# Kernel optimization log

Measured on AMD Instinct MI355X. Metric: run time of the kernel, lower is better.

Reference implementation:

```python
import jax, jax.numpy as jnp
import numpy as np

B, T, H, N = 2, 1024, 32, 64
HN = H * N              # 2048 hidden size
KVH, KVD = 8, 512       # GQA kv heads / kv width; repeat = HN // KVD = 4
LW, LA, LV, LG, LK = 64, 64, 32, 128, 32   # wavgk_split_list
EPS = 1e-6

def _rms(x, w):
    xf = x.astype(jnp.float32)
    var = jnp.mean(xf * xf, axis=-1, keepdims=True)
    return (w * (xf * jax.lax.rsqrt(var + EPS))).astype(x.dtype)

def _rot_half(x):
    x1, x2 = jnp.split(x, 2, axis=-1)
    return jnp.concatenate([-x2, x1], axis=-1)

def setup_inputs():
    key = jax.random.key(0)
    ks = iter(jax.random.split(key, 32))
    nrm = lambda s, sc=1.0: jax.random.normal(next(ks), s, jnp.float32) * sc
    d = {
        'x_in': nrm((B, T, HN)),
        'v_first': nrm((B, T, KVH, N)),
        'k_first': nrm((B, T, KVH, N)),
        'state': jnp.zeros((B, H, N, N), jnp.float32),
    }
    pos = jnp.arange(T, dtype=jnp.float32)
    inv = 1.0 / (10000.0 ** (jnp.arange(0, N, 2, dtype=jnp.float32) / N))
    ang = pos[:, None] * inv[None, :]
    ang = jnp.concatenate([ang, ang], axis=-1)   # [T, N]
    d['calc_cos'] = jnp.broadcast_to(jnp.cos(ang), (B, T, N))
    d['calc_sin'] = jnp.broadcast_to(jnp.sin(ang), (B, T, N))
    d.update(
        wavgk1=nrm((HN, LW + LA + LV + LG + LK), 0.02),
        w0=jnp.zeros((HN,), jnp.float32), w2=nrm((LW, HN), 0.02),
        a0=jnp.zeros((HN,), jnp.float32), a2=nrm((LA, HN), 0.02),
        v0=jnp.zeros((KVD,), jnp.float32), v2=nrm((LV, KVD), 0.02),
        g2=nrm((LG, HN), 0.02),
        k0=jnp.zeros((KVD,), jnp.float32), k2=nrm((LK, KVD), 0.02),
        r_k=nrm((H, N), 0.1),
        RKV_w=nrm((HN + 2 * KVD, HN), 0.02),
        O_w=nrm((HN, HN), 0.02),
        R_bias=jnp.zeros((HN,), jnp.float32),
        K_bias=jnp.zeros((KVD,), jnp.float32),
        V_bias=jnp.zeros((KVD,), jnp.float32),
        O_bias=jnp.zeros((HN,), jnp.float32),
        ln_r=jnp.ones((N,), jnp.float32),
        ln_k=jnp.ones((N,), jnp.float32),
        ln1=jnp.ones((HN,), jnp.float32),
    )
    return d

def reference(x_in, v_first, k_first, state, calc_cos, calc_sin, wavgk1, w0, w2,
              a0, a2, v0, v2, g2, k0, k2, r_k, RKV_w, O_w, R_bias, K_bias,
              V_bias, O_bias, ln_r, ln_k, ln1):
    rep = HN // KVD
    x = _rms(x_in, ln1)
    rkv = x @ RKV_w.T                                   # dense form of fpx_matmul
    r, k, v = jnp.split(rkv, [HN, HN + KVD], axis=-1)
    xw, xa, xv, xg, xk = jnp.split(x @ wavgk1, [LW, LW + LA, LW + LA + LV, LW + LA + LV + LG], axis=-1)
    r = r + R_bias; k = k + K_bias; v = v + V_bias
    r = _rms(r.reshape(B, T, H, N), ln_r)
    k = _rms(k.reshape(B, T, KVH, N), ln_k)
    cos, sin = calc_cos[:, :, None, :], calc_sin[:, :, None, :]   # unsqueeze_dim=2
    r = r * cos + _rot_half(r) * sin
    k = k * cos + _rot_half(k) * sin
    v = v.reshape(B, T, KVH, N)
    # layer_id > 0 path: gated residual toward layer-0 v/k
    gate_v = jax.nn.sigmoid(xv @ v2 + v0).reshape(B, T, KVH, N)
    v = v + (v_first - v) * gate_v
    gate_k = jax.nn.sigmoid(xk @ k2 + k0).reshape(B, T, KVH, N)
    k = k + (k_first - k) * gate_k
    w = jnp.tanh(xw) @ w2 + w0
    w = -jax.nn.softplus(-w) - 0.5
    # GQA repeat kv heads to H
    k = jnp.broadcast_to(k[:, :, :, None, :], (B, T, KVH, rep, N)).reshape(B, T, HN)
    v = jnp.broadcast_to(v[:, :, :, None, :], (B, T, KVH, rep, N)).reshape(B, T, HN)
    r = r.reshape(B, T, HN)
    a = jax.nn.sigmoid(xa @ a2 + a0)
    g = jax.nn.sigmoid(xg) @ g2
    kh = k.reshape(B, T, H, N)
    kk = (kh / jnp.maximum(jnp.linalg.norm(kh, axis=-1, keepdims=True), 1e-12)).reshape(B, T, HN)
    k = k * (1.0 - w + a)
    aa, bb = -kk, kk * a
    w = -jnp.exp(w.astype(jnp.float32))                 # log-decay (negative)
    # RWKV-7 recurrence: S <- S*diag(exp(w)) + (S a) b^T + v k^T ; o = S r
    hv = lambda t: jnp.moveaxis(t.reshape(B, T, H, N).astype(jnp.float32), 1, 0)
    def step(S, ts):
        r_t, w_t, k_t, v_t, a_t, b_t = ts               # each [B,H,N]
        sa = jnp.einsum('bhvk,bhk->bhv', S, a_t)
        S = S * jnp.exp(w_t)[:, :, None, :] + sa[..., None] * b_t[:, :, None, :] + v_t[..., None] * k_t[:, :, None, :]
        return S, jnp.einsum('bhvk,bhk->bhv', S, r_t)
    _, o = jax.lax.scan(step, state.astype(jnp.float32), (hv(r), hv(w), hv(k), hv(v), hv(aa), hv(bb)))
    xx = jnp.moveaxis(o, 0, 1).reshape(B, T, HN) * float(N) ** -0.5
    r_, k_, v_ = (t.reshape(B, T, H, N) for t in (r, k, v))
    bonus = (jnp.sum(r_ * k_ * r_k, axis=-1, keepdims=True) * v_).reshape(B, T, HN)
    xx = xx.astype(x_in.dtype) + bonus
    return x_in + (xx * g) @ O_w.T + O_bias
```

## Files before the change

### kernel.cpp

```cpp
#include <hip/hip_runtime.h>
#include <hip/hip_bf16.h>

#define B_ 2
#define T_ 1024
#define H_ 32
#define N_ 64
#define HN_ 2048
#define KVH_ 8
#define KVD_ 512
#define MTOK 2048
#define SMN 7168
#define KCAT 320
#define CH 64
#define NCH 16
#define NCHUNK 1024

typedef __bf16 bf16x8 __attribute__((ext_vector_type(8)));
typedef float f32x4 __attribute__((ext_vector_type(4)));
typedef float f32x2 __attribute__((ext_vector_type(2)));

__device__ __forceinline__ float sigmf(float x) { return 1.f / (1.f + expf(-x)); }

__global__ void f2b_kernel(const float* __restrict__ in, __hip_bfloat16* __restrict__ out, int n) {
    int i = blockIdx.x * 256 + threadIdx.x;
    if (i < n) out[i] = __float2bfloat16(in[i]);
}

__global__ void transpose_f2b_kernel(const float* __restrict__ in, __hip_bfloat16* __restrict__ out,
                                     int rows, int cols) {
    long i = (long)blockIdx.x * 256 + threadIdx.x;
    if (i >= (long)rows * cols) return;
    int c = (int)(i / rows), r = (int)(i % rows);
    out[i] = __float2bfloat16(in[(size_t)r * cols + c]);
}

__global__ void build_wcat_kernel(const float* __restrict__ w2, const float* __restrict__ a2,
                                  const float* __restrict__ v2, const float* __restrict__ g2,
                                  const float* __restrict__ k2, __hip_bfloat16* __restrict__ out) {
    long i = (long)blockIdx.x * 256 + threadIdx.x;
    if (i >= (long)SMN * KCAT) return;
    int j = (int)(i / KCAT), k = (int)(i % KCAT);
    float v = 0.f;
    if (j < 2048)      { if (k < 64)             v = w2[(size_t)k * 2048 + j]; }
    else if (j < 4096) { if (k >= 64 && k < 128)  v = a2[(size_t)(k - 64) * 2048 + (j - 2048)]; }
    else if (j < 4608) { if (k >= 128 && k < 160) v = v2[(size_t)(k - 128) * 512 + (j - 4096)]; }
    else if (j < 6656) { if (k >= 160 && k < 288) v = g2[(size_t)(k - 160) * 2048 + (j - 4608)]; }
    else               { if (k >= 288)            v = k2[(size_t)(k - 288) * 512 + (j - 6656)]; }
    out[i] = __float2bfloat16(v);
}

__global__ __launch_bounds__(256) void rmsnorm_kernel(const float* __restrict__ x,
                                                      const float* __restrict__ ln1,
                                                      __hip_bfloat16* __restrict__ out) {
    const int bt = blockIdx.x, tid = threadIdx.x;
    const float* row = x + (size_t)bt * HN_;
    float4 v0 = *(const float4*)(row + tid * 8);
    float4 v1 = *(const float4*)(row + tid * 8 + 4);
    float s = v0.x*v0.x + v0.y*v0.y + v0.z*v0.z + v0.w*v0.w
            + v1.x*v1.x + v1.y*v1.y + v1.z*v1.z + v1.w*v1.w;
    for (int m = 1; m < 64; m <<= 1) s += __shfl_xor(s, m);
    __shared__ float red[4];
    if ((tid & 63) == 0) red[tid >> 6] = s;
    __syncthreads();
    s = red[0] + red[1] + red[2] + red[3];
    float scale = rsqrtf(s * (1.f / HN_) + 1e-6f);
    float vals[8] = {v0.x, v0.y, v0.z, v0.w, v1.x, v1.y, v1.z, v1.w};
    #pragma unroll
    for (int j = 0; j < 8; ++j)
        out[(size_t)bt * HN_ + tid * 8 + j] = __float2bfloat16(vals[j] * scale * ln1[tid * 8 + j]);
}

__global__ void xwmod_kernel(const float* __restrict__ in, __hip_bfloat16* __restrict__ out) {
    long i = (long)blockIdx.x * 256 + threadIdx.x;
    if (i >= (long)MTOK * KCAT) return;
    int c = (int)(i % KCAT);
    float x = in[i];
    if (c < 64) x = tanhf(x);
    else if (c >= 160 && c < 288) x = sigmf(x);
    out[i] = __float2bfloat16(x);
}

__global__ __launch_bounds__(256) void gemm_bt(const __hip_bfloat16* __restrict__ A,
                                               const __hip_bfloat16* __restrict__ B,
                                               float* __restrict__ C, int M, int N, int K,
                                               const float* __restrict__ bias,
                                               const float* __restrict__ addend) {
    __shared__ __align__(16) __hip_bfloat16 As[64][40];
    __shared__ __align__(16) __hip_bfloat16 Bs[64][40];
    const int tid = threadIdx.x;
    const int wave = tid >> 6, lane = tid & 63;
    const int wr = (wave >> 1) * 32, wc = (wave & 1) * 32;
    const int brow = blockIdx.y << 6, bcol = blockIdx.x << 6;
    const int lrow = tid >> 2, lcol = (tid & 3) << 3;
    const int fr = lane & 15, ko = (lane >> 4) << 3;
    f32x4 acc[2][2] = {};
    for (int k0 = 0; k0 < K; k0 += 32) {
        uint4 av = *(const uint4*)(A + (size_t)(brow + lrow) * K + k0 + lcol);
        uint4 bv = *(const uint4*)(B + (size_t)(bcol + lrow) * K + k0 + lcol);
        *(uint4*)(&As[lrow][lcol]) = av;
        *(uint4*)(&Bs[lrow][lcol]) = bv;
        __syncthreads();
        bf16x8 af0 = *(const bf16x8*)(&As[wr + fr][ko]);
        bf16x8 af1 = *(const bf16x8*)(&As[wr + 16 + fr][ko]);
        bf16x8 bf0 = *(const bf16x8*)(&Bs[wc + fr][ko]);
        bf16x8 bf1 = *(const bf16x8*)(&Bs[wc + 16 + fr][ko]);
        acc[0][0] = __builtin_amdgcn_mfma_f32_16x16x32_bf16(af0, bf0, acc[0][0], 0, 0, 0);
        acc[0][1] = __builtin_amdgcn_mfma_f32_16x16x32_bf16(af0, bf1, acc[0][1], 0, 0, 0);
        acc[1][0] = __builtin_amdgcn_mfma_f32_16x16x32_bf16(af1, bf0, acc[1][0], 0, 0, 0);
        acc[1][1] = __builtin_amdgcn_mfma_f32_16x16x32_bf16(af1, bf1, acc[1][1], 0, 0, 0);
        __syncthreads();
    }
    const int cr = (lane >> 4) << 2, cc = lane & 15;
    #pragma unroll
    for (int i = 0; i < 2; ++i)
        #pragma unroll
        for (int j = 0; j < 2; ++j)
            #pragma unroll
            for (int r = 0; r < 4; ++r) {
                int row = brow + wr + i * 16 + cr + r;
                int col = bcol + wc + j * 16 + cc;
                float v = acc[i][j][r];
                if (bias) v += bias[col];
                if (addend) v += addend[(size_t)row * N + col];
                C[(size_t)row * N + col] = v;
            }
}

__global__ __launch_bounds__(256) void gemm_bt128(const __hip_bfloat16* __restrict__ A,
                                                  const __hip_bfloat16* __restrict__ B,
                                                  float* __restrict__ C, int M, int N, int K,
                                                  const float* __restrict__ bias,
                                                  const float* __restrict__ addend) {
    __shared__ __align__(16) __hip_bfloat16 As[128][40];
    __shared__ __align__(16) __hip_bfloat16 Bs[128][40];
    const int tid = threadIdx.x;
    const int wave = tid >> 6, lane = tid & 63;
    const int wr = (wave >> 1) * 64, wc = (wave & 1) * 64;
    const int brow = blockIdx.y << 7, bcol = blockIdx.x << 7;
    const int lrow = tid >> 2, lcol = (tid & 3) << 3;
    const int fr = lane & 15, ko = (lane >> 4) << 3;
    f32x4 acc[4][4] = {};
    const __hip_bfloat16* Ap = A + (size_t)(brow + lrow) * K + lcol;
    const __hip_bfloat16* Bp = B + (size_t)(bcol + lrow) * K + lcol;
    const size_t half = (size_t)64 * K;
    for (int k0 = 0; k0 < K; k0 += 32) {
        uint4 a0 = *(const uint4*)(Ap + k0);
        uint4 a1 = *(const uint4*)(Ap + half + k0);
        uint4 b0 = *(const uint4*)(Bp + k0);
        uint4 b1 = *(const uint4*)(Bp + half + k0);
        *(uint4*)(&As[lrow][lcol]) = a0;
        *(uint4*)(&As[lrow + 64][lcol]) = a1;
        *(uint4*)(&Bs[lrow][lcol]) = b0;
        *(uint4*)(&Bs[lrow + 64][lcol]) = b1;
        __syncthreads();
        bf16x8 af[4], bfr[4];
        #pragma unroll
        for (int i = 0; i < 4; ++i) {
            af[i]  = *(const bf16x8*)(&As[wr + i * 16 + fr][ko]);
            bfr[i] = *(const bf16x8*)(&Bs[wc + i * 16 + fr][ko]);
        }
        #pragma unroll
        for (int i = 0; i < 4; ++i)
            #pragma unroll
            for (int j = 0; j < 4; ++j)
                acc[i][j] = __builtin_amdgcn_mfma_f32_16x16x32_bf16(af[i], bfr[j], acc[i][j], 0, 0, 0);
        __syncthreads();
    }
    const int cr = (lane >> 4) << 2, cc = lane & 15;
    #pragma unroll
    for (int i = 0; i < 4; ++i)
        #pragma unroll
        for (int j = 0; j < 4; ++j) {
            const int row0 = brow + wr + i * 16 + cr;
            const int col = bcol + wc + j * 16 + cc;
            #pragma unroll
            for (int r = 0; r < 4; ++r) {
                float v = acc[i][j][r];
                if (bias) v += bias[col];
                if (addend) v += addend[(size_t)(row0 + r) * N + col];
                C[(size_t)(row0 + r) * N + col] = v;
            }
        }
}

__global__ __launch_bounds__(256) void compose_kernel(
    const float* __restrict__ RKV, const float* __restrict__ SM,
    const float* __restrict__ v_first, const float* __restrict__ k_first,
    const float* __restrict__ cosd, const float* __restrict__ sind,
    const float* __restrict__ R_bias, const float* __restrict__ K_bias,
    const float* __restrict__ V_bias, const float* __restrict__ w0,
    const float* __restrict__ a0, const float* __restrict__ v0b,
    const float* __restrict__ k0b, const float* __restrict__ ln_r,
    const float* __restrict__ ln_k, const float* __restrict__ r_k,
    char* __restrict__ SC, __hip_bfloat16* __restrict__ VB, float* __restrict__ SB) {
    __shared__ __align__(16) float rbuf[HN_];
    __shared__ __align__(16) float kbuf[KVD_];
    __shared__ __align__(16) float vbuf[KVD_];
    __shared__ float knorms[KVH_];
    __shared__ float cosb[64], sinb[64];
    const int bt = blockIdx.x;
    const int b = bt >> 10, t = bt & 1023;
    const int tid = threadIdx.x;
    const float* rkvrow = RKV + (size_t)bt * 3072;
    const float* smrow = SM + (size_t)bt * SMN;

    if (tid < 64) {
        cosb[tid] = cosd[(size_t)bt * 64 + tid];
        sinb[tid] = sind[(size_t)bt * 64 + tid];
    }

    const int h = tid >> 3;
    const int off = (tid & 7) << 3;
    const int n0 = tid << 3;
    float rraw[8];
    {
        float4 x0 = *(const float4*)(rkvrow + n0);
        float4 x1 = *(const float4*)(rkvrow + n0 + 4);
        float4 b0 = *(const float4*)(R_bias + n0);
        float4 b1 = *(const float4*)(R_bias + n0 + 4);
        rraw[0] = x0.x + b0.x; rraw[1] = x0.y + b0.y; rraw[2] = x0.z + b0.z; rraw[3] = x0.w + b0.w;
        rraw[4] = x1.x + b1.x; rraw[5] = x1.y + b1.y; rraw[6] = x1.z + b1.z; rraw[7] = x1.w + b1.w;
    }
    float rss = 0.f;
    #pragma unroll
    for (int j = 0; j < 8; ++j) { rss += rraw[j] * rraw[j]; rbuf[n0 + j] = rraw[j]; }
    rss += __shfl_xor(rss, 1); rss += __shfl_xor(rss, 2); rss += __shfl_xor(rss, 4);
    float rscale = rsqrtf(rss * (1.f / 64.f) + 1e-6f);

    const int kvh = tid >> 5;
    const int ko2 = (tid & 31) << 1;
    const int kidx = kvh * 64 + ko2;
    float kraw0 = rkvrow[2048 + kidx] + K_bias[kidx];
    float kraw1 = rkvrow[2048 + kidx + 1] + K_bias[kidx + 1];
    float kss = kraw0 * kraw0 + kraw1 * kraw1;
    kss += __shfl_xor(kss, 1); kss += __shfl_xor(kss, 2); kss += __shfl_xor(kss, 4);
    kss += __shfl_xor(kss, 8); kss += __shfl_xor(kss, 16);
    float kscale = rsqrtf(kss * (1.f / 64.f) + 1e-6f);
    kbuf[kidx] = kraw0; kbuf[kidx + 1] = kraw1;

    {
        float va = rkvrow[2560 + kidx] + V_bias[kidx];
        float vb2 = rkvrow[2560 + kidx + 1] + V_bias[kidx + 1];
        float gv0 = sigmf(smrow[4096 + kidx] + v0b[kidx]);
        float gv1 = sigmf(smrow[4096 + kidx + 1] + v0b[kidx + 1]);
        vbuf[kidx] = va + (v_first[(size_t)bt * 512 + kidx] - va) * gv0;
        vbuf[kidx + 1] = vb2 + (v_first[(size_t)bt * 512 + kidx + 1] - vb2) * gv1;
    }
    __syncthreads();

    float rf[8];
    #pragma unroll
    for (int j = 0; j < 8; ++j) {
        int nn = off + j;
        int nn2 = (nn + 32) & 63;
        float val = rbuf[h * 64 + nn] * rscale * ln_r[nn];
        float oth = rbuf[h * 64 + nn2] * rscale * ln_r[nn2];
        float rot = (nn < 32) ? -oth : oth;
        rf[j] = val * cosb[nn] + rot * sinb[nn];
    }
    float kfv[2];
    #pragma unroll
    for (int j = 0; j < 2; ++j) {
        int nn = ko2 + j;
        int nn2 = (nn + 32) & 63;
        float val = kbuf[kvh * 64 + nn] * kscale * ln_k[nn];
        float oth = kbuf[kvh * 64 + nn2] * kscale * ln_k[nn2];
        float rot = (nn < 32) ? -oth : oth;
        float kr = val * cosb[nn] + rot * sinb[nn];
        float gk = sigmf(smrow[6656 + kvh * 64 + nn] + k0b[kvh * 64 + nn]);
        kfv[j] = kr + (k_first[(size_t)bt * 512 + kvh * 64 + nn] - kr) * gk;
    }
    __syncthreads();
    kbuf[kidx] = kfv[0]; kbuf[kidx + 1] = kfv[1];
    float kn = kfv[0] * kfv[0] + kfv[1] * kfv[1];
    kn += __shfl_xor(kn, 1); kn += __shfl_xor(kn, 2); kn += __shfl_xor(kn, 4);
    kn += __shfl_xor(kn, 8); kn += __shfl_xor(kn, 16);
    if ((tid & 31) == 0) knorms[kvh] = fmaxf(sqrtf(kn), 1e-12f);
    __syncthreads();

    const float knv = knorms[h >> 2];
    char* scb = SC + ((size_t)(b * H_ + h) * T_ + t) * 896;
    __hip_bfloat16* us = (__hip_bfloat16*)scb;
    float* df = (float*)(scb + 640);
    float4 w1a = *(const float4*)(smrow + n0);
    float4 w1b = *(const float4*)(smrow + n0 + 4);
    float4 ara = *(const float4*)(smrow + 2048 + n0);
    float4 arb = *(const float4*)(smrow + 2048 + n0 + 4);
    float w1arr[8] = {w1a.x, w1a.y, w1a.z, w1a.w, w1b.x, w1b.y, w1b.z, w1b.w};
    float aarr[8] = {ara.x, ara.y, ara.z, ara.w, arb.x, arb.y, arb.z, arb.w};
    float bsum = 0.f;
    #pragma unroll
    for (int j = 0; j < 8; ++j) {
        int nn = off + j, n = n0 + j;
        float w1 = w1arr[j] + w0[n];
        float w2v = -log1pf(expf(-w1)) - 0.5f;
        float av = sigmf(aarr[j] + a0[n]);
        float dec = expf(-expf(w2v));
        float kb = kbuf[(h >> 2) * 64 + nn];
        float vbv = vbuf[(h >> 2) * 64 + nn];
        float kkv = kb / knv;
        float ksc = kb * (1.f - w2v + av);
        us[nn]       = __float2bfloat16(rf[j]);
        us[64 + nn]  = __float2bfloat16(ksc);
        us[128 + nn] = __float2bfloat16(-kkv);
        us[192 + nn] = __float2bfloat16(kkv * av);
        us[256 + nn] = __float2bfloat16(vbv);
        df[nn] = dec;
        VB[(size_t)bt * HN_ + n] = __float2bfloat16(vbv);
        bsum += rf[j] * ksc * r_k[h * 64 + nn];
    }
    bsum += __shfl_xor(bsum, 1); bsum += __shfl_xor(bsum, 2); bsum += __shfl_xor(bsum, 4);
    if ((tid & 7) == 0) SB[bt * H_ + h] = bsum;
}

__global__ __launch_bounds__(256) void scan_pass1(
    const char* __restrict__ SC, float* __restrict__ Q, float* __restrict__ O,
    float* __restrict__ Pf, float* __restrict__ Sf) {
    const int chunk = blockIdx.x;
    const int bh = chunk >> 4, c = chunk & 15;
    const int b = bh >> 5, h = bh & 31;
    const int tid = threadIdx.x;
    const int wid = tid >> 6, lane = tid & 63;
    const int mat = wid >> 1;
    const int rhalf = wid & 1;
    const int row = rhalf * 32 + (lane & 31);
    const int chalf = lane >> 5;
    const int cb = chalf * 32;
    const char* base = SC + ((size_t)bh * T_ + (size_t)c * CH) * 896;
    __shared__ __align__(16) float ld[2][5][64];

    f32x4 R4[8];
    #pragma unroll
    for (int j = 0; j < 8; ++j)
        #pragma unroll
        for (int e = 0; e < 4; ++e)
            R4[j][e] = (mat == 0 && cb + 4 * j + e == row) ? 1.f : 0.f;

    float p0, p1;
    auto LOADT = [&](int t) {
        const __hip_bfloat16* us = (const __hip_bfloat16*)(base + (size_t)t * 896);
        if (wid == 0)      { p0 = __bfloat162float(us[128 + lane]); p1 = __bfloat162float(us[lane]); }
        else if (wid == 1) { p0 = __bfloat162float(us[192 + lane]); p1 = 0.f; }
        else if (wid == 2) { p0 = *(const float*)(base + (size_t)t * 896 + 640 + 4 * lane);
                             p1 = __bfloat162float(us[256 + (lane & 31)]); }
        else               { p0 = __bfloat162float(us[64 + lane]);
                             p1 = __bfloat162float(us[256 + 32 + (lane & 31)]); }
    };
    LOADT(0);
    float* qrow = Q + (size_t)chunk * CH * 64 + row;
    float* orow = O + ((size_t)b * T_ + (size_t)c * CH) * HN_ + h * 64 + row;
    for (int t = 0; t < CH; ++t) {
        const int buf = t & 1;
        float vt = p1;
        if (wid == 0)      { ld[buf][0][lane] = p0; ld[buf][4][lane] = p1; }
        else if (wid == 1) { ld[buf][1][lane] = p0; }
        else if (wid == 2) { ld[buf][2][lane] = p0; }
        else               { ld[buf][3][lane] = p0; }
        __syncthreads();
        if (t + 1 < CH) LOADT(t + 1);
        f32x4 da = {0,0,0,0}, db = {0,0,0,0};
        #pragma unroll
        for (int j = 0; j < 8; j += 2) {
            da += R4[j]     * *(const f32x4*)&ld[buf][0][cb + 4 * j];
            db += R4[j + 1] * *(const f32x4*)&ld[buf][0][cb + 4 * j + 4];
        }
        float dot = da[0] + da[1] + da[2] + da[3] + db[0] + db[1] + db[2] + db[3];
        dot += __shfl_xor(dot, 32);
        const f32x4 dotv = {dot, dot, dot, dot};
        f32x4 qa = {0,0,0,0}, qb = {0,0,0,0};
        if (mat == 0) {
            #pragma unroll
            for (int j = 0; j < 8; j += 2) {
                f32x4 d0 = *(const f32x4*)&ld[buf][2][cb + 4 * j];
                f32x4 b0 = *(const f32x4*)&ld[buf][1][cb + 4 * j];
                f32x4 r0 = *(const f32x4*)&ld[buf][4][cb + 4 * j];
                f32x4 Pn = R4[j] * d0 + dotv * b0;
                R4[j] = Pn; qa += Pn * r0;
                f32x4 d1 = *(const f32x4*)&ld[buf][2][cb + 4 * j + 4];
                f32x4 b1 = *(const f32x4*)&ld[buf][1][cb + 4 * j + 4];
                f32x4 r1 = *(const f32x4*)&ld[buf][4][cb + 4 * j + 4];
                f32x4 Pm = R4[j + 1] * d1 + dotv * b1;
                R4[j + 1] = Pm; qb += Pm * r1;
            }
            float qs = qa[0]+qa[1]+qa[2]+qa[3]+qb[0]+qb[1]+qb[2]+qb[3];
            qs += __shfl_xor(qs, 32);
            if (chalf == 0) qrow[(size_t)t * 64] = qs;
        } else {
            const f32x4 vtv = {vt, vt, vt, vt};
            #pragma unroll
            for (int j = 0; j < 8; j += 2) {
                f32x4 d0 = *(const f32x4*)&ld[buf][2][cb + 4 * j];
                f32x4 b0 = *(const f32x4*)&ld[buf][1][cb + 4 * j];
                f32x4 k0 = *(const f32x4*)&ld[buf][3][cb + 4 * j];
                f32x4 r0 = *(const f32x4*)&ld[buf][4][cb + 4 * j];
                f32x4 Sn = R4[j] * d0 + dotv * b0 + vtv * k0;
                R4[j] = Sn; qa += Sn * r0;
                f32x4 d1 = *(const f32x4*)&ld[buf][2][cb + 4 * j + 4];
                f32x4 b1 = *(const f32x4*)&ld[buf][1][cb + 4 * j + 4];
                f32x4 k1 = *(const f32x4*)&ld[buf][3][cb + 4 * j + 4];
                f32x4 r1 = *(const f32x4*)&ld[buf][4][cb + 4 * j + 4];
                f32x4 Sm = R4[j + 1] * d1 + dotv * b1 + vtv * k1;
                R4[j + 1] = Sm; qb += Sm * r1;
            }
            float os = qa[0]+qa[1]+qa[2]+qa[3]+qb[0]+qb[1]+qb[2]+qb[3];
            os += __shfl_xor(os, 32);
            if (chalf == 0) orow[(size_t)t * HN_] = os;
        }
    }
    float* fp = (mat == 0 ? Pf : Sf) + (size_t)chunk * 4096 + (size_t)row * 64 + cb;
    #pragma unroll
    for (int j = 0; j < 8; ++j)
        *(f32x4*)(fp + 4 * j) = R4[j];
}

__global__ __launch_bounds__(256) void scan_pass2(
    const float* __restrict__ Pf, float* __restrict__ Sf, const float* __restrict__ state) {
    const int blk = blockIdx.x;
    const int bh = blk >> 2, rb = blk & 3;
    const int tid = threadIdx.x;
    const int lv = tid >> 4, c0 = (tid & 15) << 2;
    __shared__ __align__(16) float S[16][68];
    __shared__ __align__(16) float P[64][64];

    *(f32x4*)&S[lv][c0] = *(const f32x4*)&state[(size_t)bh * 4096 + 1024 * rb + tid * 4];
    const size_t pbase = (size_t)(bh * NCH) * 4096;
    {
        f32x4 p0[4];
        #pragma unroll
        for (int j = 0; j < 4; ++j) p0[j] = *(const f32x4*)&Pf[pbase + tid * 16 + 4 * j];
        #pragma unroll
        for (int j = 0; j < 4; ++j) *(f32x4*)(&P[0][0] + tid * 16 + 4 * j) = p0[j];
    }
    __syncthreads();

    for (int c = 0; c < NCH; ++c) {
        const size_t ck = (size_t)(bh * NCH + c) * 4096;
        f32x4 pp[4];
        if (c + 1 < NCH) {
            #pragma unroll
            for (int j = 0; j < 4; ++j) pp[j] = *(const f32x4*)&Pf[ck + 4096 + tid * 16 + 4 * j];
        }
        f32x4 acc = *(const f32x4*)&Sf[ck + 1024 * rb + tid * 4];
        f32x4 cur = *(const f32x4*)&S[lv][c0];
        #pragma unroll 4
        for (int k4 = 0; k4 < 64; k4 += 4) {
            f32x4 sk4 = *(const f32x4*)&S[lv][k4];
            #pragma unroll
            for (int kk = 0; kk < 4; ++kk) {
                f32x4 pr = *(const f32x4*)&P[k4 + kk][c0];
                f32x4 sv = {sk4[kk], sk4[kk], sk4[kk], sk4[kk]};
                acc += sv * pr;
            }
        }
        __syncthreads();
        *(f32x4*)&S[lv][c0] = acc;
        if (c + 1 < NCH) {
            #pragma unroll
            for (int j = 0; j < 4; ++j) *(f32x4*)(&P[0][0] + tid * 16 + 4 * j) = pp[j];
        }
        *(f32x4*)&Sf[ck + 1024 * rb + tid * 4] = cur;
        __syncthreads();
    }
}

__global__ __launch_bounds__(64) void scan_pass3(
    const float* __restrict__ Q, const float* __restrict__ Sinit, float* __restrict__ O) {
    const int chunk = blockIdx.x;
    const int bh = chunk >> 4, c = chunk & 15;
    const int b = bh >> 5, h = bh & 31;
    const int t = threadIdx.x;
    __shared__ __align__(16) float S[64][64];
    #pragma unroll
    for (int j = 0; j < 16; ++j)
        *(f32x4*)&S[t][4 * j] = *(const f32x4*)&Sinit[(size_t)chunk * 4096 + (size_t)t * 64 + 4 * j];
    __syncthreads();
    float q[64];
    #pragma unroll
    for (int j = 0; j < 16; ++j)
        *(f32x4*)&q[4 * j] = *(const f32x4*)&Q[((size_t)chunk * CH + t) * 64 + 4 * j];
    float* orow = O + ((size_t)b * T_ + (size_t)c * CH + t) * HN_ + h * 64;
    #pragma unroll 4
    for (int v = 0; v < 64; ++v) {
        f32x4 a = {0, 0, 0, 0};
        #pragma unroll
        for (int j = 0; j < 16; ++j)
            a += *(const f32x4*)&S[v][4 * j] * *(const f32x4*)&q[4 * j];
        orow[v] = (a[0] + a[1] + a[2] + a[3] + orow[v]) * 0.125f;
    }
}

__global__ void post_kernel(const float* __restrict__ O, const float* __restrict__ SB,
                            const __hip_bfloat16* __restrict__ VB, const float* __restrict__ SM,
                            __hip_bfloat16* __restrict__ Ub) {
    long i = (long)blockIdx.x * 256 + threadIdx.x;
    if (i >= (long)MTOK * HN_) return;
    int bt = (int)(i >> 11), n = (int)(i & 2047), h = n >> 6;
    float u = (O[i] + SB[bt * H_ + h] * __bfloat162float(VB[i])) * SM[(size_t)bt * SMN + 4608 + n];
    Ub[i] = __float2bfloat16(u);
}

extern "C" void kernel_launch(void* const* d_in, const int* in_sizes, int n_in,
                              void* d_out, int out_size, void* d_ws, size_t ws_size,
                              hipStream_t stream) {
    (void)in_sizes; (void)n_in; (void)out_size; (void)ws_size;
    const float* x_in    = (const float*)d_in[0];
    const float* v_first = (const float*)d_in[1];
    const float* k_first = (const float*)d_in[2];
    const float* state   = (const float*)d_in[3];
    const float* calc_cos= (const float*)d_in[4];
    const float* calc_sin= (const float*)d_in[5];
    const float* wavgk1  = (const float*)d_in[6];
    const float* w0      = (const float*)d_in[7];
    const float* w2      = (const float*)d_in[8];
    const float* a0      = (const float*)d_in[9];
    const float* a2      = (const float*)d_in[10];
    const float* v0      = (const float*)d_in[11];
    const float* v2      = (const float*)d_in[12];
    const float* g2      = (const float*)d_in[13];
    const float* k0      = (const float*)d_in[14];
    const float* k2      = (const float*)d_in[15];
    const float* r_k     = (const float*)d_in[16];
    const float* RKV_w   = (const float*)d_in[17];
    const float* O_w     = (const float*)d_in[18];
    const float* R_bias  = (const float*)d_in[19];
    const float* K_bias  = (const float*)d_in[20];
    const float* V_bias  = (const float*)d_in[21];
    const float* O_bias  = (const float*)d_in[22];
    const float* ln_r    = (const float*)d_in[23];
    const float* ln_k    = (const float*)d_in[24];
    const float* ln1     = (const float*)d_in[25];
    float* out = (float*)d_out;

    char* ws = (char*)d_ws;
    size_t off = 0;
    auto alloc = [&](size_t bytes) -> char* {
        char* p = ws + off;
        off = (off + bytes + 255) & ~(size_t)255;
        return p;
    };
    float* SMf = (float*)alloc((size_t)MTOK * SMN * 4);
    char*  SCb = alloc((size_t)64 * T_ * 896);
    __hip_bfloat16* Ub = (__hip_bfloat16*)SCb;
    __hip_bfloat16* VBb = (__hip_bfloat16*)alloc((size_t)MTOK * HN_ * 2);
    float* SBf = (float*)alloc((size_t)MTOK * H_ * 4);
    float* Of  = (float*)alloc((size_t)MTOK * HN_ * 4);
    __hip_bfloat16* OWb = (__hip_bfloat16*)alloc((size_t)2048 * 2048 * 2);

    size_t ovl = off;
    __hip_bfloat16* Xb     = (__hip_bfloat16*)alloc((size_t)MTOK * HN_ * 2);
    __hip_bfloat16* RKVb   = (__hip_bfloat16*)alloc((size_t)3072 * 2048 * 2);
    __hip_bfloat16* WT1b   = (__hip_bfloat16*)alloc((size_t)320 * 2048 * 2);
    __hip_bfloat16* Wcatb  = (__hip_bfloat16*)alloc((size_t)SMN * KCAT * 2);
    __hip_bfloat16* XWmodb = (__hip_bfloat16*)alloc((size_t)MTOK * KCAT * 2);
    float* RKVf  = (float*)alloc((size_t)MTOK * 3072 * 4);
    float* XWraw = (float*)alloc((size_t)MTOK * KCAT * 4);
    off = ovl;
    float* Qf  = (float*)alloc((size_t)NCHUNK * CH * 64 * 4);
    float* Pff = (float*)alloc((size_t)NCHUNK * 4096 * 4);
    float* Sff = (float*)alloc((size_t)NCHUNK * 4096 * 4);

    f2b_kernel<<<(3072 * 2048 + 255) / 256, 256, 0, stream>>>(RKV_w, RKVb, 3072 * 2048);
    f2b_kernel<<<(2048 * 2048 + 255) / 256, 256, 0, stream>>>(O_w, OWb, 2048 * 2048);
    transpose_f2b_kernel<<<(320 * 2048 + 255) / 256, 256, 0, stream>>>(wavgk1, WT1b, 2048, 320);
    build_wcat_kernel<<<(SMN * KCAT + 255) / 256, 256, 0, stream>>>(w2, a2, v2, g2, k2, Wcatb);

    rmsnorm_kernel<<<MTOK, 256, 0, stream>>>(x_in, ln1, Xb);

    gemm_bt128<<<dim3(3072 / 128, MTOK / 128), 256, 0, stream>>>(Xb, RKVb, RKVf, MTOK, 3072, 2048, nullptr, nullptr);
    gemm_bt<<<dim3(320 / 64, MTOK / 64), 256, 0, stream>>>(Xb, WT1b, XWraw, MTOK, 320, 2048, nullptr, nullptr);
    xwmod_kernel<<<(MTOK * KCAT + 255) / 256, 256, 0, stream>>>(XWraw, XWmodb);
    gemm_bt128<<<dim3(SMN / 128, MTOK / 128), 256, 0, stream>>>(XWmodb, Wcatb, SMf, MTOK, SMN, KCAT, nullptr, nullptr);

    compose_kernel<<<MTOK, 256, 0, stream>>>(RKVf, SMf, v_first, k_first, calc_cos, calc_sin,
                                             R_bias, K_bias, V_bias, w0, a0, v0, k0,
                                             ln_r, ln_k, r_k, SCb, VBb, SBf);

    scan_pass1<<<NCHUNK, 256, 0, stream>>>(SCb, Qf, Of, Pff, Sff);
    scan_pass2<<<B_ * H_ * 4, 256, 0, stream>>>(Pff, Sff, state);
    scan_pass3<<<NCHUNK, 64, 0, stream>>>(Qf, Sff, Of);

    post_kernel<<<(MTOK * HN_ + 255) / 256, 256, 0, stream>>>(Of, SBf, VBb, SMf, Ub);
    gemm_bt128<<<dim3(HN_ / 128, MTOK / 128), 256, 0, stream>>>(Ub, OWb, out, MTOK, HN_, 2048, O_bias, x_in);
}
```

Before: 459.0 us.

## Halve scan chunk size, merge prep kernels, fuse pass3 with post gating

Scan chunk length drops from 64 to 32, doubling the number of chunks so more blocks run in the parallel scan passes. The four weight-conversion kernels are merged into one prep launch. The gate values are written as bf16 by the compose kernel, so the SM buffer can move into the overlapped workspace region. The separate post kernel is folded into scan pass3, which now produces the gated bf16 output directly, removing one full pass over the fp32 output. The trade-off is more per-chunk state traffic in pass1, pass2 and pass3, and an extra bf16 gate buffer.

```diff
diff --git a/kernel.cpp b/kernel.cpp
--- a/kernel.cpp
+++ b/kernel.cpp
@@ -11,9 +11,9 @@
 #define MTOK 2048
 #define SMN 7168
 #define KCAT 320
-#define CH 64
-#define NCH 16
-#define NCHUNK 1024
+#define CH 32
+#define NCH 32
+#define NCHUNK 2048
 
 typedef __bf16 bf16x8 __attribute__((ext_vector_type(8)));
 typedef float f32x4 __attribute__((ext_vector_type(4)));
@@ -21,24 +21,29 @@
 
 __device__ __forceinline__ float sigmf(float x) { return 1.f / (1.f + expf(-x)); }
 
-__global__ void f2b_kernel(const float* __restrict__ in, __hip_bfloat16* __restrict__ out, int n) {
-    int i = blockIdx.x * 256 + threadIdx.x;
-    if (i < n) out[i] = __float2bfloat16(in[i]);
-}
-
-__global__ void transpose_f2b_kernel(const float* __restrict__ in, __hip_bfloat16* __restrict__ out,
-                                     int rows, int cols) {
+#define PREP_N1 (3072 * 2048)
+#define PREP_N2 (2048 * 2048)
+#define PREP_N3 (320 * 2048)
+#define PREP_N4 (SMN * KCAT)
+__global__ void prep_kernel(const float* __restrict__ RKV_w, const float* __restrict__ O_w,
+                            const float* __restrict__ wavgk1,
+                            const float* __restrict__ w2, const float* __restrict__ a2,
+                            const float* __restrict__ v2, const float* __restrict__ g2,
+                            const float* __restrict__ k2,
+                            __hip_bfloat16* __restrict__ RKVb, __hip_bfloat16* __restrict__ OWb,
+                            __hip_bfloat16* __restrict__ WT1b, __hip_bfloat16* __restrict__ Wcatb) {
     long i = (long)blockIdx.x * 256 + threadIdx.x;
-    if (i >= (long)rows * cols) return;
-    int c = (int)(i / rows), r = (int)(i % rows);
-    out[i] = __float2bfloat16(in[(size_t)r * cols + c]);
-}
-
-__global__ void build_wcat_kernel(const float* __restrict__ w2, const float* __restrict__ a2,
-                                  const float* __restrict__ v2, const float* __restrict__ g2,
-                                  const float* __restrict__ k2, __hip_bfloat16* __restrict__ out) {
-    long i = (long)blockIdx.x * 256 + threadIdx.x;
-    if (i >= (long)SMN * KCAT) return;
+    if (i < PREP_N1) { RKVb[i] = __float2bfloat16(RKV_w[i]); return; }
+    i -= PREP_N1;
+    if (i < PREP_N2) { OWb[i] = __float2bfloat16(O_w[i]); return; }
+    i -= PREP_N2;
+    if (i < PREP_N3) {
+        int c = (int)(i / 2048), r = (int)(i % 2048);
+        WT1b[i] = __float2bfloat16(wavgk1[(size_t)r * 320 + c]);
+        return;
+    }
+    i -= PREP_N3;
+    if (i >= PREP_N4) return;
     int j = (int)(i / KCAT), k = (int)(i % KCAT);
     float v = 0.f;
     if (j < 2048)      { if (k < 64)             v = w2[(size_t)k * 2048 + j]; }
@@ -46,7 +51,7 @@
     else if (j < 4608) { if (k >= 128 && k < 160) v = v2[(size_t)(k - 128) * 512 + (j - 4096)]; }
     else if (j < 6656) { if (k >= 160 && k < 288) v = g2[(size_t)(k - 160) * 2048 + (j - 4608)]; }
     else               { if (k >= 288)            v = k2[(size_t)(k - 288) * 512 + (j - 6656)]; }
-    out[i] = __float2bfloat16(v);
+    Wcatb[i] = __float2bfloat16(v);
 }
 
 __global__ __launch_bounds__(256) void rmsnorm_kernel(const float* __restrict__ x,
@@ -192,7 +197,8 @@
     const float* __restrict__ a0, const float* __restrict__ v0b,
     const float* __restrict__ k0b, const float* __restrict__ ln_r,
     const float* __restrict__ ln_k, const float* __restrict__ r_k,
-    char* __restrict__ SC, __hip_bfloat16* __restrict__ VB, float* __restrict__ SB) {
+    char* __restrict__ SC, __hip_bfloat16* __restrict__ VB, float* __restrict__ SB,
+    __hip_bfloat16* __restrict__ G) {
     __shared__ __align__(16) float rbuf[HN_];
     __shared__ __align__(16) float kbuf[KVD_];
     __shared__ __align__(16) float vbuf[KVD_];
@@ -286,8 +292,11 @@
     float4 w1b = *(const float4*)(smrow + n0 + 4);
     float4 ara = *(const float4*)(smrow + 2048 + n0);
     float4 arb = *(const float4*)(smrow + 2048 + n0 + 4);
+    float4 ga  = *(const float4*)(smrow + 4608 + n0);
+    float4 gb  = *(const float4*)(smrow + 4608 + n0 + 4);
     float w1arr[8] = {w1a.x, w1a.y, w1a.z, w1a.w, w1b.x, w1b.y, w1b.z, w1b.w};
     float aarr[8] = {ara.x, ara.y, ara.z, ara.w, arb.x, arb.y, arb.z, arb.w};
+    float garr[8] = {ga.x, ga.y, ga.z, ga.w, gb.x, gb.y, gb.z, gb.w};
     float bsum = 0.f;
     #pragma unroll
     for (int j = 0; j < 8; ++j) {
@@ -307,6 +316,7 @@
         us[256 + nn] = __float2bfloat16(vbv);
         df[nn] = dec;
         VB[(size_t)bt * HN_ + n] = __float2bfloat16(vbv);
+        G[(size_t)bt * HN_ + n] = __float2bfloat16(garr[j]);
         bsum += rf[j] * ksc * r_k[h * 64 + nn];
     }
     bsum += __shfl_xor(bsum, 1); bsum += __shfl_xor(bsum, 2); bsum += __shfl_xor(bsum, 4);
@@ -317,7 +327,7 @@
     const char* __restrict__ SC, float* __restrict__ Q, float* __restrict__ O,
     float* __restrict__ Pf, float* __restrict__ Sf) {
     const int chunk = blockIdx.x;
-    const int bh = chunk >> 4, c = chunk & 15;
+    const int bh = chunk >> 5, c = chunk & 31;
     const int b = bh >> 5, h = bh & 31;
     const int tid = threadIdx.x;
     const int wid = tid >> 6, lane = tid & 63;
@@ -463,40 +473,41 @@
     }
 }
 
-__global__ __launch_bounds__(64) void scan_pass3(
-    const float* __restrict__ Q, const float* __restrict__ Sinit, float* __restrict__ O) {
+__global__ __launch_bounds__(64) void pass3_post(
+    const float* __restrict__ Q, const float* __restrict__ Sinit, const float* __restrict__ OL,
+    const float* __restrict__ SB, const __hip_bfloat16* __restrict__ VB,
+    const __hip_bfloat16* __restrict__ G, __hip_bfloat16* __restrict__ Ub) {
     const int chunk = blockIdx.x;
-    const int bh = chunk >> 4, c = chunk & 15;
+    const int bh = chunk >> 5, c = chunk & 31;
     const int b = bh >> 5, h = bh & 31;
-    const int t = threadIdx.x;
+    const int tid = threadIdx.x;
     __shared__ __align__(16) float S[64][64];
     #pragma unroll
     for (int j = 0; j < 16; ++j)
-        *(f32x4*)&S[t][4 * j] = *(const f32x4*)&Sinit[(size_t)chunk * 4096 + (size_t)t * 64 + 4 * j];
+        *(f32x4*)&S[tid][4 * j] = *(const f32x4*)&Sinit[(size_t)chunk * 4096 + (size_t)tid * 64 + 4 * j];
     __syncthreads();
+    const int t = tid >> 1, vh = (tid & 1) << 5;
+    const size_t bt = (size_t)b * T_ + (size_t)c * CH + t;
     float q[64];
     #pragma unroll
     for (int j = 0; j < 16; ++j)
         *(f32x4*)&q[4 * j] = *(const f32x4*)&Q[((size_t)chunk * CH + t) * 64 + 4 * j];
-    float* orow = O + ((size_t)b * T_ + (size_t)c * CH + t) * HN_ + h * 64;
+    const float sb = SB[bt * H_ + h];
+    const float* olrow = OL + bt * HN_ + h * 64;
+    const __hip_bfloat16* vbrow = VB + bt * HN_ + h * 64;
+    const __hip_bfloat16* grow = G + bt * HN_ + h * 64;
+    __hip_bfloat16* urow = Ub + bt * HN_ + h * 64;
     #pragma unroll 4
-    for (int v = 0; v < 64; ++v) {
+    for (int v = 0; v < 32; ++v) {
+        const int vv = vh + v;
         f32x4 a = {0, 0, 0, 0};
         #pragma unroll
         for (int j = 0; j < 16; ++j)
-            a += *(const f32x4*)&S[v][4 * j] * *(const f32x4*)&q[4 * j];
-        orow[v] = (a[0] + a[1] + a[2] + a[3] + orow[v]) * 0.125f;
-    }
-}
-
-__global__ void post_kernel(const float* __restrict__ O, const float* __restrict__ SB,
-                            const __hip_bfloat16* __restrict__ VB, const float* __restrict__ SM,
-                            __hip_bfloat16* __restrict__ Ub) {
-    long i = (long)blockIdx.x * 256 + threadIdx.x;
-    if (i >= (long)MTOK * HN_) return;
-    int bt = (int)(i >> 11), n = (int)(i & 2047), h = n >> 6;
-    float u = (O[i] + SB[bt * H_ + h] * __bfloat162float(VB[i])) * SM[(size_t)bt * SMN + 4608 + n];
-    Ub[i] = __float2bfloat16(u);
+            a += *(const f32x4*)&S[vv][4 * j] * *(const f32x4*)&q[4 * j];
+        float o = (a[0] + a[1] + a[2] + a[3] + olrow[vv]) * 0.125f;
+        float u = (o + sb * __bfloat162float(vbrow[vv])) * __bfloat162float(grow[vv]);
+        urow[vv] = __float2bfloat16(u);
+    }
 }
 
 extern "C" void kernel_launch(void* const* d_in, const int* in_sizes, int n_in,
@@ -538,15 +549,16 @@
         off = (off + bytes + 255) & ~(size_t)255;
         return p;
     };
-    float* SMf = (float*)alloc((size_t)MTOK * SMN * 4);
     char*  SCb = alloc((size_t)64 * T_ * 896);
     __hip_bfloat16* Ub = (__hip_bfloat16*)SCb;
     __hip_bfloat16* VBb = (__hip_bfloat16*)alloc((size_t)MTOK * HN_ * 2);
+    __hip_bfloat16* Gb  = (__hip_bfloat16*)alloc((size_t)MTOK * HN_ * 2);
     float* SBf = (float*)alloc((size_t)MTOK * H_ * 4);
     float* Of  = (float*)alloc((size_t)MTOK * HN_ * 4);
     __hip_bfloat16* OWb = (__hip_bfloat16*)alloc((size_t)2048 * 2048 * 2);
 
     size_t ovl = off;
+    float* SMf = (float*)alloc((size_t)MTOK * SMN * 4);
     __hip_bfloat16* Xb     = (__hip_bfloat16*)alloc((size_t)MTOK * HN_ * 2);
     __hip_bfloat16* RKVb   = (__hip_bfloat16*)alloc((size_t)3072 * 2048 * 2);
     __hip_bfloat16* WT1b   = (__hip_bfloat16*)alloc((size_t)320 * 2048 * 2);
@@ -559,10 +571,11 @@
     float* Pff = (float*)alloc((size_t)NCHUNK * 4096 * 4);
     float* Sff = (float*)alloc((size_t)NCHUNK * 4096 * 4);
 
-    f2b_kernel<<<(3072 * 2048 + 255) / 256, 256, 0, stream>>>(RKV_w, RKVb, 3072 * 2048);
-    f2b_kernel<<<(2048 * 2048 + 255) / 256, 256, 0, stream>>>(O_w, OWb, 2048 * 2048);
-    transpose_f2b_kernel<<<(320 * 2048 + 255) / 256, 256, 0, stream>>>(wavgk1, WT1b, 2048, 320);
-    build_wcat_kernel<<<(SMN * KCAT + 255) / 256, 256, 0, stream>>>(w2, a2, v2, g2, k2, Wcatb);
+    {
+        long total = (long)PREP_N1 + PREP_N2 + PREP_N3 + PREP_N4;
+        prep_kernel<<<(int)((total + 255) / 256), 256, 0, stream>>>(
+            RKV_w, O_w, wavgk1, w2, a2, v2, g2, k2, RKVb, OWb, WT1b, Wcatb);
+    }
 
     rmsnorm_kernel<<<MTOK, 256, 0, stream>>>(x_in, ln1, Xb);
 
@@ -573,12 +586,11 @@
 
     compose_kernel<<<MTOK, 256, 0, stream>>>(RKVf, SMf, v_first, k_first, calc_cos, calc_sin,
                                              R_bias, K_bias, V_bias, w0, a0, v0, k0,
-                                             ln_r, ln_k, r_k, SCb, VBb, SBf);
+                                             ln_r, ln_k, r_k, SCb, VBb, SBf, Gb);
 
     scan_pass1<<<NCHUNK, 256, 0, stream>>>(SCb, Qf, Of, Pff, Sff);
     scan_pass2<<<B_ * H_ * 4, 256, 0, stream>>>(Pff, Sff, state);
-    scan_pass3<<<NCHUNK, 64, 0, stream>>>(Qf, Sff, Of);
-
-    post_kernel<<<(MTOK * HN_ + 255) / 256, 256, 0, stream>>>(Of, SBf, VBb, SMf, Ub);
+    pass3_post<<<NCHUNK, 64, 0, stream>>>(Qf, Sff, Of, SBf, VBb, Gb, Ub);
+
     gemm_bt128<<<dim3(HN_ / 128, MTOK / 128), 256, 0, stream>>>(Ub, OWb, out, MTOK, HN_, 2048, O_bias, x_in);
 }
```

After: 511.0 us. 11.3% more time.
